# Optimization experiments

Measured on AMD Instinct MI355X. Metric: run time of the kernel, lower is better.

The kernel has to match this reference:

```python
import jax, jax.numpy as jnp
import numpy as np
from jax import lax

B, C, H, W = 4, 256, 64, 64
R1, R2 = 4, 8


def conv1x1(x, w, b):
    # x: [B,C,H,W], w: [O,C], b: [O]
    return jnp.einsum('bchw,oc->bohw', x, w) + b[None, :, None, None]


def dwconv3x3(x, w, b):
    # depthwise 3x3, SAME padding. w: [C,1,3,3]
    y = lax.conv_general_dilated(x, w, window_strides=(1, 1), padding='SAME',
                                 dimension_numbers=('NCHW', 'OIHW', 'NCHW'),
                                 feature_group_count=x.shape[1])
    return y + b[None, :, None, None]


def setup_inputs() -> dict:
    key = jax.random.key(0)
    ks = jax.random.split(key, 20)
    s = 0.02
    inp = {
        'x':   jax.random.normal(ks[0], (B, C, H, W), jnp.float32),
        'Wq':  jax.random.normal(ks[1], (C, C), jnp.float32) * s,
        'bq':  jnp.zeros((C,), jnp.float32),
        'Wk':  jax.random.normal(ks[2], (C, 1, 3, 3), jnp.float32) * s,
        'bk':  jnp.zeros((C,), jnp.float32),
        'Wv':  jax.random.normal(ks[3], (C, 1, 3, 3), jnp.float32) * s,
        'bv':  jnp.zeros((C,), jnp.float32),
        'Wl':  jax.random.normal(ks[4], (C, 1, 3, 3), jnp.float32) * s,
        'bl':  jnp.zeros((C,), jnp.float32),
        'Ws1': jax.random.normal(ks[5], (C // R1, C), jnp.float32) * s,
        'bs1': jnp.zeros((C // R1,), jnp.float32),
        'Ws2': jax.random.normal(ks[6], (C, C // R1), jnp.float32) * s,
        'bs2': jnp.zeros((C,), jnp.float32),
        'Wc1': jax.random.normal(ks[7], (C // R2, C), jnp.float32) * s,
        'bc1': jnp.zeros((C // R2,), jnp.float32),
        'Wc2': jax.random.normal(ks[8], (C, C // R2), jnp.float32) * s,
        'bc2': jnp.zeros((C,), jnp.float32),
        'Wo':  jax.random.normal(ks[9], (C, C), jnp.float32) * s,
        'bo':  jnp.zeros((C,), jnp.float32),
    }
    return inp


def reference(x, Wq, bq, Wk, bk, Wv, bv, Wl, bl, Ws1, bs1, Ws2, bs2,
              Wc1, bc1, Wc2, bc2, Wo, bo):
    b_, c_, h_, w_ = x.shape
    hw = h_ * w_
    scale = jnp.sqrt(jnp.float32(c_))

    q = conv1x1(x, Wq, bq).reshape(b_, c_, hw).transpose(0, 2, 1)   # [B,HW,C]
    k = dwconv3x3(x, Wk, bk).reshape(b_, c_, hw)                    # [B,C,HW]
    v_img = dwconv3x3(x, Wv, bv)                                    # [B,C,H,W]
    v = v_img.reshape(b_, c_, hw).transpose(0, 2, 1)                # [B,HW,C]

    attn = jax.nn.softmax(jnp.einsum('bnc,bcm->bnm', q, k) / scale, axis=-1)
    global_out = jnp.einsum('bnm,bmc->bnc', attn, v)                # [B,HW,C]
    global_out = global_out.transpose(0, 2, 1).reshape(b_, c_, h_, w_)

    local_out = dwconv3x3(v_img, Wl, bl)                            # [B,C,H,W]

    spatial_weight = jax.nn.sigmoid(
        conv1x1(jax.nn.relu(conv1x1(local_out, Ws1, bs1)), Ws2, bs2))

    gap = jnp.mean(global_out, axis=(2, 3), keepdims=True)          # [B,C,1,1]
    channel_weight = jax.nn.sigmoid(
        conv1x1(jax.nn.relu(conv1x1(gap, Wc1, bc1)), Wc2, bc2))     # [B,C,1,1]

    fused = global_out * channel_weight + local_out * spatial_weight
    return conv1x1(fused, Wo, bo) + x
```

## Files before the change

### kernel.cpp

```cpp
#include <hip/hip_runtime.h>
#include <hip/hip_fp8.h>
#include <stdint.h>

typedef unsigned short u16;
typedef unsigned char u8;
typedef __attribute__((ext_vector_type(8))) __bf16 bf16x8;
typedef __attribute__((ext_vector_type(8))) short short8s;
typedef __attribute__((ext_vector_type(4))) float float4v;
typedef __attribute__((ext_vector_type(16))) float floatx16;

static constexpr int NB = 4, NC = 256, NH = 64, NW = 64, NHW = 4096;
static constexpr int BC = 64;
static constexpr int NKV = 4;
static constexpr int KVCHUNK = NHW / NKV;

static constexpr size_t MB = 1ull << 20;
static constexpr size_t OFF_KBF    = 0;
static constexpr size_t OFF_LBF    = 8 * MB;
static constexpr size_t OFF_GT     = 0;
static constexpr size_t OFF_XT     = 16 * MB;
static constexpr size_t OFF_LPART  = 16 * MB;
static constexpr size_t OFF_FUSEDT = 16 * MB;
static constexpr size_t OFF_QT8    = 24 * MB;
static constexpr size_t OFF_KT8    = 32 * MB;
static constexpr size_t OFF_V8     = 40 * MB;
static constexpr size_t OFF_LT     = 48 * MB;
static constexpr size_t OFF_OPART  = 56 * MB;
static constexpr size_t OFF_HIDT   = 88 * MB;
static constexpr size_t OFF_GAP    = OFF_HIDT + 2 * MB;
static constexpr size_t OFF_WQB    = OFF_GAP + 8 * 1024;
static constexpr size_t OFF_WS1B   = OFF_WQB + 131072;
static constexpr size_t OFF_WS2B   = OFF_WS1B + 32768;
static constexpr size_t OFF_WOB    = OFF_WS2B + 32768;

__device__ __forceinline__ float b2f(u16 h) {
    union { float f; unsigned u; } v; v.u = ((unsigned)h) << 16; return v.f;
}
__device__ __forceinline__ u16 f2b(float f) {
    union { float f; unsigned u; } v; v.f = f;
    unsigned r = v.u + 0x7fffu + ((v.u >> 16) & 1u);
    return (u16)(r >> 16);
}
__device__ __forceinline__ u8 f2f8(float f) {
    __hip_fp8_e4m3 h(f);
    return *reinterpret_cast<u8*>(&h);
}

__device__ __forceinline__ void load_lds16(const void* gsrc, void* ldst) {
    __builtin_amdgcn_global_load_lds(
        (__attribute__((address_space(1))) void*)(uintptr_t)gsrc,
        (__attribute__((address_space(3))) void*)ldst,
        16, 0, 0);
}

__global__ __launch_bounds__(256) void prep(
    const float* __restrict__ x,
    const float* __restrict__ Wq, const float* __restrict__ Ws1,
    const float* __restrict__ Ws2, const float* __restrict__ Wo,
    const float* __restrict__ Wk, const float* __restrict__ bk,
    const float* __restrict__ Wv, const float* __restrict__ bv,
    const float* __restrict__ Wl, const float* __restrict__ bl,
    u16* __restrict__ Wqb, u16* __restrict__ Ws1b, u16* __restrict__ Ws2b, u16* __restrict__ Wob,
    float* __restrict__ gap,
    u16* __restrict__ k_bf, u8* __restrict__ vN8, u16* __restrict__ local_bf,
    u16* __restrict__ xT)
{
    __shared__ __align__(16) unsigned char pshm[9216];
    const int bid = blockIdx.x;
    const int t = threadIdx.x;

    if (bid < 644) {
        int id = bid * 256 + t;
        if (id < 65536)        Wqb[id] = f2b(Wq[id]);
        else if (id < 81920)   Ws1b[id - 65536] = f2b(Ws1[id - 65536]);
        else if (id < 98304)   Ws2b[id - 81920] = f2b(Ws2[id - 81920]);
        else if (id < 163840)  Wob[id - 98304] = f2b(Wo[id - 98304]);
        else if (id < 164864)  gap[id - 163840] = 0.f;
        return;
    }
    if (bid < 2692) {
        int l = bid - 644;
        int xx0 = t & 63, cl = t >> 6;
        int y0 = (l & 7) * 8;
        int c  = ((l >> 3) & 63) * 4 + cl;
        int b  = l >> 9;
        const float* xb = x + ((size_t)b * NC + c) * NHW;
        float wk[9], wv[9], wl[9];
#pragma unroll
        for (int i = 0; i < 9; i++) { wk[i] = Wk[c*9+i]; wv[i] = Wv[c*9+i]; wl[i] = Wl[c*9+i]; }
        float bkc = bk[c], bvc = bv[c], blc = bl[c];

        auto ldx = [&](int y) -> float {
            return ((unsigned)y <= 63u) ? xb[y * 64 + xx0] : 0.f;
        };
        auto conv3 = [&](const float* w9, float a, float bm, float cc) -> float {
            float au = __shfl_up(a, 1, 64),   ad = __shfl_down(a, 1, 64);
            float bu = __shfl_up(bm, 1, 64),  bd = __shfl_down(bm, 1, 64);
            float cu = __shfl_up(cc, 1, 64),  cd = __shfl_down(cc, 1, 64);
            float al = (xx0 == 0) ? 0.f : au, ar = (xx0 == 63) ? 0.f : ad;
            float bl_ = (xx0 == 0) ? 0.f : bu, br = (xx0 == 63) ? 0.f : bd;
            float cle = (xx0 == 0) ? 0.f : cu, cr = (xx0 == 63) ? 0.f : cd;
            return w9[0]*al + w9[1]*a  + w9[2]*ar
                 + w9[3]*bl_ + w9[4]*bm + w9[5]*br
                 + w9[6]*cle + w9[7]*cc + w9[8]*cr;
        };

        float xm2 = ldx(y0 - 2), xm1 = ldx(y0 - 1), x0v = ldx(y0), xp1 = ldx(y0 + 1);
        float vm1 = (y0 - 1 >= 0) ? (bvc + conv3(wv, xm2, xm1, x0v)) : 0.f;
        float v0  = bvc + conv3(wv, xm1, x0v, xp1);

        size_t base = ((size_t)b * NC + c) * NHW;
#pragma unroll
        for (int yi = 0; yi < 8; yi++) {
            int y = y0 + yi;
            float xp2 = ldx(y + 2);
            float vp1 = (y + 1 <= 63) ? (bvc + conv3(wv, x0v, xp1, xp2)) : 0.f;
            float kk  = bkc + conv3(wk, xm1, x0v, xp1);
            float ll  = blc + conv3(wl, vm1, v0, vp1);
            size_t o = base + y * 64 + xx0;
            k_bf[o]     = f2b(kk);
            vN8[o]      = f2f8(v0);
            local_bf[o] = f2b(ll);
            xm1 = x0v; x0v = xp1; xp1 = xp2;
            vm1 = v0;  v0 = vp1;
        }
        return;
    }
    {
        u16 (*tile)[72] = reinterpret_cast<u16 (*)[72]>(pshm);
        int l = bid - 2692;
        int n0 = (l & 63) * 64;
        int c0 = ((l >> 6) & 3) * 64;
        int b  = l >> 8;
        const float* src = x + (size_t)b * NC * NHW;
        u16* dst = xT + (size_t)b * NHW * NC;
        int c = t >> 2, nb = (t & 3) * 16;
#pragma unroll
        for (int q = 0; q < 4; q++) {
            float4 v = *(const float4*)(src + (size_t)(c0 + c) * NHW + n0 + nb + q * 4);
            tile[c][nb + q * 4 + 0] = f2b(v.x);
            tile[c][nb + q * 4 + 1] = f2b(v.y);
            tile[c][nb + q * 4 + 2] = f2b(v.z);
            tile[c][nb + q * 4 + 3] = f2b(v.w);
        }
        __syncthreads();
        int cl = t & 63, ng = t >> 6;
#pragma unroll
        for (int j = 0; j < 16; j++) {
            int n = ng * 16 + j;
            dst[(size_t)(n0 + n) * NC + c0 + cl] = tile[cl][n];
        }
    }
}

__global__ __launch_bounds__(256) void mid(
    const u16* __restrict__ k_bf, const u16* __restrict__ local_bf,
    u8* __restrict__ kT8, u16* __restrict__ localT,
    const u16* __restrict__ xT, const u16* __restrict__ Wqb, const float* __restrict__ bq,
    u8* __restrict__ qT8)
{
    __shared__ __align__(16) u16 tile[64][72];
    const int t = threadIdx.x;
    const int bid = blockIdx.x;
    if (bid < 2048) {
        int n0 = (bid & 63) * 64, c0 = ((bid >> 6) & 3) * 64;
        int zb = bid >> 8, b = zb >> 1;
        const u16* src = (zb & 1) ? local_bf : k_bf;
        src += (size_t)b * NC * NHW;
        int c = t >> 2, nb = (t & 3) * 16;
        *(short8s*)&tile[c][nb]     = *(const short8s*)(src + (size_t)(c0 + c) * NHW + n0 + nb);
        *(short8s*)&tile[c][nb + 8] = *(const short8s*)(src + (size_t)(c0 + c) * NHW + n0 + nb + 8);
        __syncthreads();
        int cl = t & 63, ng = t >> 6;
        if (zb & 1) {
            u16* dst = localT + (size_t)b * NHW * NC;
#pragma unroll
            for (int j = 0; j < 16; j++) {
                int n = ng * 16 + j;
                dst[(size_t)(n0 + n) * NC + c0 + cl] = tile[cl][n];
            }
        } else {
            u8* dst = kT8 + (size_t)b * NHW * NC;
#pragma unroll
            for (int j = 0; j < 16; j++) {
                int n = ng * 16 + j;
                dst[(size_t)(n0 + n) * NC + c0 + cl] = f2f8(b2f(tile[cl][n]));
            }
        }
        return;
    }
    {
        const int w = t >> 6, lane = t & 63;
        const int lm = lane & 15, quad = lane >> 4;
        const int l = bid - 2048;
        const int b = l >> 7;
        const int s_base = (l & 127) * 32 + (w & 1) * 16;
        const int ch = (w >> 1) * 128;
        const u16* xTb = xT + (size_t)b * NHW * NC;
        u8* qTb = qT8 + (size_t)b * NHW * NC;
        bf16x8 aq[8];
#pragma unroll
        for (int kt = 0; kt < 8; kt++)
            aq[kt] = *(const bf16x8*)(xTb + (size_t)(s_base + lm) * NC + kt * 32 + quad * 8);
        float4v acc[8];
#pragma unroll
        for (int j = 0; j < 8; j++) acc[j] = (float4v){0.f, 0.f, 0.f, 0.f};
#pragma unroll
        for (int kt = 0; kt < 8; kt++) {
#pragma unroll
            for (int j = 0; j < 8; j++) {
                bf16x8 bw = *(const bf16x8*)(Wqb + (size_t)(ch + j * 16 + lm) * 256 + kt * 32 + quad * 8);
                acc[j] = __builtin_amdgcn_mfma_f32_16x16x32_bf16(aq[kt], bw, acc[j], 0, 0, 0);
            }
        }
#pragma unroll
        for (int j = 0; j < 8; j++) {
            int cout = ch + j * 16 + lm;
            float bb = bq[cout];
#pragma unroll
            for (int r = 0; r < 4; r++) {
                int s = s_base + quad * 4 + r;
                qTb[(size_t)s * NC + cout] = f2f8(acc[j][r] + bb);
            }
        }
    }
}

__device__ __forceinline__ void stage_tiles(
    const u8* __restrict__ kb, const u8* __restrict__ vb8, int kv0,
    u8* KlB, u8* VlB, int w, int lane)
{
#pragma unroll
    for (int i = 0; i < 4; i++) {
        int g = (w * 4 + i) * 64 + lane;
        int n = g >> 4, jj = g & 15, cc = jj ^ (n & 15);
        load_lds16(kb + (size_t)(kv0 + n) * NC + cc * 16, KlB + (w * 4 + i) * 1024);
    }
#pragma unroll
    for (int i = 0; i < 4; i++) {
        int g = (w * 4 + i) * 64 + lane;
        int c = g >> 2, hh = g & 3;
        int sc = hh ^ ((c >> 1) & 3);
        load_lds16(vb8 + (size_t)c * NHW + kv0 + sc * 16, VlB + (w * 4 + i) * 1024);
    }
}

__global__ __launch_bounds__(256, 2) void attn_hid(
    const u8* __restrict__ qT8, const u8* __restrict__ kT8,
    const u8* __restrict__ vN8, u8* __restrict__ Opart8, float* __restrict__ lpart,
    const u16* __restrict__ localT, const u16* __restrict__ Ws1b, const float* __restrict__ bs1,
    u16* __restrict__ hidT)
{
    __shared__ __align__(16) u8 Kl[2][BC * 256];
    __shared__ __align__(16) u8 Vl[2][256 * BC];

    const int t = threadIdx.x;
    const int w = t >> 6, lane = t & 63;

    if (blockIdx.x >= 512) {
        const int lm = lane & 15, quad = lane >> 4;
        const int l = blockIdx.x - 512;
        const int b = l >> 7;
        const int s_base = (l & 127) * 32 + (w & 1) * 16;
        const int ch = (w >> 1) * 32;
        const u16* lTb = localT + (size_t)b * NHW * NC;
        u16* hTb = hidT + (size_t)b * NHW * 64;
        bf16x8 ah[8];
#pragma unroll
        for (int kt = 0; kt < 8; kt++)
            ah[kt] = *(const bf16x8*)(lTb + (size_t)(s_base + lm) * NC + kt * 32 + quad * 8);
        float4v acc[2];
#pragma unroll
        for (int j = 0; j < 2; j++) acc[j] = (float4v){0.f, 0.f, 0.f, 0.f};
#pragma unroll
        for (int kt = 0; kt < 8; kt++) {
#pragma unroll
            for (int j = 0; j < 2; j++) {
                bf16x8 bw = *(const bf16x8*)(Ws1b + (size_t)(ch + j * 16 + lm) * 256 + kt * 32 + quad * 8);
                acc[j] = __builtin_amdgcn_mfma_f32_16x16x32_bf16(ah[kt], bw, acc[j], 0, 0, 0);
            }
        }
#pragma unroll
        for (int j = 0; j < 2; j++) {
            int h = ch + j * 16 + lm;
            float bb = bs1[h];
#pragma unroll
            for (int r = 0; r < 4; r++) {
                int s = s_base + quad * 4 + r;
                hTb[(size_t)s * 64 + h] = f2b(fmaxf(acc[j][r] + bb, 0.0f));
            }
        }
        return;
    }

    const int combo = blockIdx.x & 15;
    const int b  = combo >> 2;
    const int jc = combo & 3;
    const int n0 = (blockIdx.x >> 4) * 128;
    const int lr = lane & 31, l5 = lane >> 5;

    const u8* qb = qT8 + (size_t)b * NHW * NC;
    const u8* kb = kT8 + (size_t)b * NHW * NC;
    const u8* vb8 = vN8 + (size_t)b * NC * NHW;

    long aq[16];
    {
        int qrow = n0 + w * 32 + lr;
#pragma unroll
        for (int kt = 0; kt < 16; kt++)
            aq[kt] = *(const long*)(qb + (size_t)qrow * NC + kt * 16 + l5 * 8);
    }

    floatx16 oacc[8];
#pragma unroll
    for (int i = 0; i < 8; i++)
#pragma unroll
        for (int j = 0; j < 16; j++) oacc[i][j] = 0.f;
    float lsum = 0.f;

    const int kvbeg = jc * KVCHUNK;
    stage_tiles(kb, vb8, kvbeg, Kl[0], Vl[0], w, lane);

    int buf = 0;
#pragma unroll 1
    for (int it = 0; it < KVCHUNK / BC; it++) {
        const int nxt = (it + 1 < KVCHUNK / BC) ? (kvbeg + (it + 1) * BC) : kvbeg;
        stage_tiles(kb, vb8, nxt, Kl[buf ^ 1], Vl[buf ^ 1], w, lane);
        asm volatile("s_waitcnt vmcnt(8)" ::: "memory");
        __builtin_amdgcn_s_barrier();

        const u8* KlB = Kl[buf];
        const u8* VlB = Vl[buf];

#pragma unroll
        for (int s = 0; s < 2; s++) {
            floatx16 sacc;
#pragma unroll
            for (int j = 0; j < 16; j++) sacc[j] = 0.f;
            __builtin_amdgcn_s_setprio(1);
#pragma unroll
            for (int kt = 0; kt < 16; kt++) {
                long ak = *(const long*)&KlB[(s * 32 + lr) * 256 + ((kt ^ (lr & 15)) * 16) + l5 * 8];
                sacc = __builtin_amdgcn_mfma_f32_32x32x16_fp8_fp8(ak, aq[kt], sacc, 0, 0, 0);
            }
            __builtin_amdgcn_s_setprio(0);
            unsigned u0 = 0, u1 = 0, u2 = 0, u3 = 0;
            {
                float p[16];
#pragma unroll
                for (int r = 0; r < 16; r++)
                    p[r] = __expf(sacc[r] * 0.0625f);
                float s0 = (p[0] + p[1]) + (p[2] + p[3]);
                float s1 = (p[4] + p[5]) + (p[6] + p[7]);
                float s2 = (p[8] + p[9]) + (p[10] + p[11]);
                float s3 = (p[12] + p[13]) + (p[14] + p[15]);
                lsum += (s0 + s1) + (s2 + s3);
                u0 = __builtin_amdgcn_cvt_pk_fp8_f32(p[0], p[1], 0, false);
                u0 = __builtin_amdgcn_cvt_pk_fp8_f32(p[2], p[3], u0, true);
                u1 = __builtin_amdgcn_cvt_pk_fp8_f32(p[4], p[5], 0, false);
                u1 = __builtin_amdgcn_cvt_pk_fp8_f32(p[6], p[7], u1, true);
                u2 = __builtin_amdgcn_cvt_pk_fp8_f32(p[8], p[9], 0, false);
                u2 = __builtin_amdgcn_cvt_pk_fp8_f32(p[10], p[11], u2, true);
                u3 = __builtin_amdgcn_cvt_pk_fp8_f32(p[12], p[13], 0, false);
                u3 = __builtin_amdgcn_cvt_pk_fp8_f32(p[14], p[15], u3, true);
            }
            asm volatile("v_permlane32_swap_b32 %0, %1" : "+v"(u0), "+v"(u1));
            asm volatile("v_permlane32_swap_b32 %0, %1" : "+v"(u2), "+v"(u3));
            long A1 = (long)(((unsigned long long)u1 << 32) | u0);
            long A2 = (long)(((unsigned long long)u3 << 32) | u2);

            __builtin_amdgcn_s_setprio(1);
#pragma unroll
            for (int ct = 0; ct < 8; ct++) {
                int c = ct * 32 + lr;
                int sw = (c >> 1) & 3;
                long bv0 = *(const long*)&VlB[c * 64 + (((2 * s) ^ sw) * 16) + l5 * 8];
                long bv1 = *(const long*)&VlB[c * 64 + (((2 * s + 1) ^ sw) * 16) + l5 * 8];
                oacc[ct] = __builtin_amdgcn_mfma_f32_32x32x16_fp8_fp8(A1, bv0, oacc[ct], 0, 0, 0);
                oacc[ct] = __builtin_amdgcn_mfma_f32_32x32x16_fp8_fp8(A2, bv1, oacc[ct], 0, 0, 0);
            }
            __builtin_amdgcn_s_setprio(0);
        }
        __builtin_amdgcn_s_barrier();
        buf ^= 1;
    }

    lsum += __shfl_xor(lsum, 32, 64);
    u8* Ob = Opart8 + ((size_t)(b * NKV + jc) * NHW + n0 + w * 32) * NC;
#pragma unroll
    for (int reg = 0; reg < 16; reg++) {
        int row = (reg & 3) + 8 * (reg >> 2) + 4 * l5;
#pragma unroll
        for (int ct = 0; ct < 8; ct++)
            Ob[(size_t)row * NC + ct * 32 + lr] = f2f8(oacc[ct][reg]);
    }
    if (lane < 32)
        lpart[(size_t)(b * NKV + jc) * NHW + n0 + w * 32 + lr] = lsum;
}

__global__ __launch_bounds__(256) void attn_combine(
    const u8* __restrict__ Opart8, const float* __restrict__ lpart,
    u16* __restrict__ gT, float* __restrict__ gap)
{
    __shared__ float gsum[256];
    int t = threadIdx.x;
    gsum[t] = 0.f;
    __syncthreads();
    int b = blockIdx.y;
    int n = blockIdx.x * 8 + (t >> 5);
    int c0 = (t & 31) * 8;
    float acc[8] = {};
    float l = 0.f;
#pragma unroll
    for (int j = 0; j < NKV; j++) {
        const u8* op = Opart8 + ((size_t)(b * NKV + j) * NHW + n) * NC + c0;
        unsigned long long v = *(const unsigned long long*)op;
        unsigned lo = (unsigned)v, hi = (unsigned)(v >> 32);
        acc[0] += __builtin_amdgcn_cvt_f32_fp8(lo, 0);
        acc[1] += __builtin_amdgcn_cvt_f32_fp8(lo, 1);
        acc[2] += __builtin_amdgcn_cvt_f32_fp8(lo, 2);
        acc[3] += __builtin_amdgcn_cvt_f32_fp8(lo, 3);
        acc[4] += __builtin_amdgcn_cvt_f32_fp8(hi, 0);
        acc[5] += __builtin_amdgcn_cvt_f32_fp8(hi, 1);
        acc[6] += __builtin_amdgcn_cvt_f32_fp8(hi, 2);
        acc[7] += __builtin_amdgcn_cvt_f32_fp8(hi, 3);
        l += lpart[(size_t)(b * NKV + j) * NHW + n];
    }
    float inv = 1.0f / l;
#pragma unroll
    for (int i = 0; i < 8; i++) acc[i] *= inv;
    short8s vo;
#pragma unroll
    for (int i = 0; i < 8; i++) ((u16*)&vo)[i] = f2b(acc[i]);
    *(short8s*)(gT + ((size_t)b * NHW + n) * NC + c0) = vo;
#pragma unroll
    for (int i = 0; i < 8; i++) atomicAdd(&gsum[c0 + i], acc[i]);
    __syncthreads();
    atomicAdd(&gap[b * NC + t], gsum[t]);
}

__global__ __launch_bounds__(256) void gemm_swfused_mfma(
    const u16* __restrict__ hidT, const u16* __restrict__ Ws2b, const float* __restrict__ bs2,
    const u16* __restrict__ gT, const u16* __restrict__ localT,
    const float* __restrict__ gap,
    const float* __restrict__ Wc1, const float* __restrict__ bc1,
    const float* __restrict__ Wc2, const float* __restrict__ bc2,
    u16* __restrict__ fusedT)
{
    __shared__ float g[256], h1[32], cwl[256];
    __shared__ float ph[32][9];
    const int t = threadIdx.x, w = t >> 6, lane = t & 63;
    const int lm = lane & 15, quad = lane >> 4;
    const int b = blockIdx.y;

    g[t] = gap[b * 256 + t] * (1.0f / 4096.0f);
    __syncthreads();
    {
        int h = t & 31, part = t >> 5;
        float s = 0.f;
        for (int c = part * 32; c < part * 32 + 32; c++) s += Wc1[h * 256 + c] * g[c];
        ph[h][part] = s;
    }
    __syncthreads();
    if (t < 32) {
        float s = bc1[t];
#pragma unroll
        for (int p = 0; p < 8; p++) s += ph[t][p];
        h1[t] = fmaxf(s, 0.f);
    }
    __syncthreads();
    {
        float s = bc2[t];
#pragma unroll
        for (int j = 0; j < 32; j++) s += Wc2[t * 32 + j] * h1[j];
        cwl[t] = 1.0f / (1.0f + __expf(-s));
    }
    __syncthreads();

    const int s_base = blockIdx.x * 32 + (w & 1) * 16;
    const int ch = (w >> 1) * 128;
    const u16* hTb = hidT + (size_t)b * NHW * 64;
    const u16* lTb = localT + (size_t)b * NHW * NC;
    const u16* gTb = gT + (size_t)b * NHW * NC;
    u16* fTb = fusedT + (size_t)b * NHW * NC;

    bf16x8 aq[2];
#pragma unroll
    for (int kt = 0; kt < 2; kt++)
        aq[kt] = *(const bf16x8*)(hTb + (size_t)(s_base + lm) * 64 + kt * 32 + quad * 8);

    float4v acc[8];
#pragma unroll
    for (int j = 0; j < 8; j++) acc[j] = (float4v){0.f, 0.f, 0.f, 0.f};

#pragma unroll
    for (int kt = 0; kt < 2; kt++) {
#pragma unroll
        for (int j = 0; j < 8; j++) {
            bf16x8 bw = *(const bf16x8*)(Ws2b + (size_t)(ch + j * 16 + lm) * 64 + kt * 32 + quad * 8);
            acc[j] = __builtin_amdgcn_mfma_f32_16x16x32_bf16(aq[kt], bw, acc[j], 0, 0, 0);
        }
    }
#pragma unroll
    for (int j = 0; j < 8; j++) {
        int c = ch + j * 16 + lm;
        float bb = bs2[c];
        float cwv = cwl[c];
#pragma unroll
        for (int r = 0; r < 4; r++) {
            int s = s_base + quad * 4 + r;
            float sw = 1.0f / (1.0f + __expf(-(acc[j][r] + bb)));
            float gg = b2f(gTb[(size_t)s * NC + c]);
            float lo = b2f(lTb[(size_t)s * NC + c]);
            fTb[(size_t)s * NC + c] = f2b(gg * cwv + lo * sw);
        }
    }
}

__global__ __launch_bounds__(256) void gemm_out_mfma(
    const u16* __restrict__ Wob, const u16* __restrict__ fusedT, const float* __restrict__ bo,
    const float* __restrict__ x, float* __restrict__ out)
{
    const int t = threadIdx.x, w = t >> 6, lane = t & 63;
    const int lm = lane & 15, quad = lane >> 4;
    const int b = blockIdx.z;
    const int o_base = blockIdx.x * 32 + (w & 1) * 16;
    const int n_base = blockIdx.y * 256 + (w >> 1) * 128;
    const u16* fTb = fusedT + (size_t)b * NHW * NC;

    bf16x8 aw[8];
#pragma unroll
    for (int kt = 0; kt < 8; kt++)
        aw[kt] = *(const bf16x8*)(Wob + (size_t)(o_base + lm) * 256 + kt * 32 + quad * 8);

    float4v acc[8];
#pragma unroll
    for (int j = 0; j < 8; j++) acc[j] = (float4v){0.f, 0.f, 0.f, 0.f};

#pragma unroll
    for (int kt = 0; kt < 8; kt++) {
#pragma unroll
        for (int j = 0; j < 8; j++) {
            bf16x8 bf = *(const bf16x8*)(fTb + (size_t)(n_base + j * 16 + lm) * NC + kt * 32 + quad * 8);
            acc[j] = __builtin_amdgcn_mfma_f32_16x16x32_bf16(aw[kt], bf, acc[j], 0, 0, 0);
        }
    }
#pragma unroll
    for (int r = 0; r < 4; r++) {
        int o = o_base + quad * 4 + r;
        float bb = bo[o];
        size_t rowoff = ((size_t)b * NC + o) * NHW;
#pragma unroll
        for (int j = 0; j < 8; j++) {
            int n = n_base + j * 16 + lm;
            out[rowoff + n] = acc[j][r] + bb + x[rowoff + n];
        }
    }
}

extern "C" void kernel_launch(void* const* d_in, const int* in_sizes, int n_in,
                              void* d_out, int out_size, void* d_ws, size_t ws_size,
                              hipStream_t stream)
{
    const float* x   = (const float*)d_in[0];
    const float* Wq  = (const float*)d_in[1];
    const float* bq  = (const float*)d_in[2];
    const float* Wk  = (const float*)d_in[3];
    const float* bk  = (const float*)d_in[4];
    const float* Wv  = (const float*)d_in[5];
    const float* bv  = (const float*)d_in[6];
    const float* Wl  = (const float*)d_in[7];
    const float* bl  = (const float*)d_in[8];
    const float* Ws1 = (const float*)d_in[9];
    const float* bs1 = (const float*)d_in[10];
    const float* Ws2 = (const float*)d_in[11];
    const float* bs2 = (const float*)d_in[12];
    const float* Wc1 = (const float*)d_in[13];
    const float* bc1 = (const float*)d_in[14];
    const float* Wc2 = (const float*)d_in[15];
    const float* bc2 = (const float*)d_in[16];
    const float* Wo  = (const float*)d_in[17];
    const float* bo  = (const float*)d_in[18];
    float* out = (float*)d_out;

    char* ws = (char*)d_ws;
    u16* k_bf     = (u16*)(ws + OFF_KBF);
    u16* local_bf = (u16*)(ws + OFF_LBF);
    u16* gT       = (u16*)(ws + OFF_GT);
    u16* xT       = (u16*)(ws + OFF_XT);
    u16* fusedT   = (u16*)(ws + OFF_FUSEDT);
    u8*  qT8      = (u8*)(ws + OFF_QT8);
    u8*  kT8      = (u8*)(ws + OFF_KT8);
    u8*  vN8      = (u8*)(ws + OFF_V8);
    u16* localT   = (u16*)(ws + OFF_LT);
    u8*  Opart8   = (u8*)(ws + OFF_OPART);
    float* lpart  = (float*)(ws + OFF_LPART);
    u16* hidT     = (u16*)(ws + OFF_HIDT);
    float* gap    = (float*)(ws + OFF_GAP);
    u16* Wqb      = (u16*)(ws + OFF_WQB);
    u16* Ws1b     = (u16*)(ws + OFF_WS1B);
    u16* Ws2b     = (u16*)(ws + OFF_WS2B);
    u16* Wob      = (u16*)(ws + OFF_WOB);

    prep<<<dim3(3716), 256, 0, stream>>>(x, Wq, Ws1, Ws2, Wo, Wk, bk, Wv, bv, Wl, bl,
                                         Wqb, Ws1b, Ws2b, Wob, gap, k_bf, vN8, local_bf, xT);
    mid<<<dim3(2560), 256, 0, stream>>>(k_bf, local_bf, kT8, localT, xT, Wqb, bq, qT8);
    attn_hid<<<dim3(1024), 256, 0, stream>>>(qT8, kT8, vN8, Opart8, lpart,
                                             localT, Ws1b, bs1, hidT);
    attn_combine<<<dim3(NHW / 8, 4), 256, 0, stream>>>(Opart8, lpart, gT, gap);
    gemm_swfused_mfma<<<dim3(128, 4), 256, 0, stream>>>(hidT, Ws2b, bs2, gT, localT,
                                                        gap, Wc1, bc1, Wc2, bc2, fusedT);
    gemm_out_mfma<<<dim3(8, 16, 4), 256, 0, stream>>>(Wob, fusedT, bo, x, out);
}
```

Measured before the change: 274.3 us.

## Use scaled 32x32x64 fp8 MFMA for attention QK and PV products

New measurement: 259.9 us. 5.3% less time.

```diff
diff --git a/kernel.cpp b/kernel.cpp
--- a/kernel.cpp
+++ b/kernel.cpp
@@ -8,6 +8,8 @@
 typedef __attribute__((ext_vector_type(8))) short short8s;
 typedef __attribute__((ext_vector_type(4))) float float4v;
 typedef __attribute__((ext_vector_type(16))) float floatx16;
+typedef __attribute__((ext_vector_type(4))) int int4v;
+typedef __attribute__((ext_vector_type(8))) int int8v;
 
 static constexpr int NB = 4, NC = 256, NH = 64, NW = 64, NHW = 4096;
 static constexpr int BC = 64;
@@ -298,17 +300,19 @@
     const int jc = combo & 3;
     const int n0 = (blockIdx.x >> 4) * 128;
     const int lr = lane & 31, l5 = lane >> 5;
+    const int m4 = lr & 15;
+    const int scl = (int)0x7F7F7F7F;
 
     const u8* qb = qT8 + (size_t)b * NHW * NC;
     const u8* kb = kT8 + (size_t)b * NHW * NC;
     const u8* vb8 = vN8 + (size_t)b * NC * NHW;
 
-    long aq[16];
+    int8v aqm[4];
     {
         int qrow = n0 + w * 32 + lr;
 #pragma unroll
-        for (int kt = 0; kt < 16; kt++)
-            aq[kt] = *(const long*)(qb + (size_t)qrow * NC + kt * 16 + l5 * 8);
+        for (int ks = 0; ks < 4; ks++)
+            aqm[ks] = *(const int8v*)(qb + (size_t)qrow * NC + ks * 64 + l5 * 32);
     }
 
     floatx16 oacc[8];
@@ -332,55 +336,93 @@
         const u8* KlB = Kl[buf];
         const u8* VlB = Vl[buf];
 
-#pragma unroll
-        for (int s = 0; s < 2; s++) {
+        unsigned uA0, uA1, uA2, uA3, uB0, uB1, uB2, uB3;
+
+        {
             floatx16 sacc;
 #pragma unroll
             for (int j = 0; j < 16; j++) sacc[j] = 0.f;
             __builtin_amdgcn_s_setprio(1);
 #pragma unroll
-            for (int kt = 0; kt < 16; kt++) {
-                long ak = *(const long*)&KlB[(s * 32 + lr) * 256 + ((kt ^ (lr & 15)) * 16) + l5 * 8];
-                sacc = __builtin_amdgcn_mfma_f32_32x32x16_fp8_fp8(ak, aq[kt], sacc, 0, 0, 0);
+            for (int ks = 0; ks < 4; ks++) {
+                int e = ks * 4 + l5 * 2;
+                int4v klo = *(const int4v*)&KlB[lr * 256 + ((e ^ m4) * 16)];
+                int4v khi = *(const int4v*)&KlB[lr * 256 + (((e + 1) ^ m4) * 16)];
+                int8v ka = __builtin_shufflevector(klo, khi, 0, 1, 2, 3, 4, 5, 6, 7);
+                sacc = __builtin_amdgcn_mfma_scale_f32_32x32x64_f8f6f4(
+                    ka, aqm[ks], sacc, 0, 0, 0, scl, 0, scl);
             }
             __builtin_amdgcn_s_setprio(0);
-            unsigned u0 = 0, u1 = 0, u2 = 0, u3 = 0;
-            {
-                float p[16];
-#pragma unroll
-                for (int r = 0; r < 16; r++)
-                    p[r] = __expf(sacc[r] * 0.0625f);
-                float s0 = (p[0] + p[1]) + (p[2] + p[3]);
-                float s1 = (p[4] + p[5]) + (p[6] + p[7]);
-                float s2 = (p[8] + p[9]) + (p[10] + p[11]);
-                float s3 = (p[12] + p[13]) + (p[14] + p[15]);
-                lsum += (s0 + s1) + (s2 + s3);
-                u0 = __builtin_amdgcn_cvt_pk_fp8_f32(p[0], p[1], 0, false);
-                u0 = __builtin_amdgcn_cvt_pk_fp8_f32(p[2], p[3], u0, true);
-                u1 = __builtin_amdgcn_cvt_pk_fp8_f32(p[4], p[5], 0, false);
-                u1 = __builtin_amdgcn_cvt_pk_fp8_f32(p[6], p[7], u1, true);
-                u2 = __builtin_amdgcn_cvt_pk_fp8_f32(p[8], p[9], 0, false);
-                u2 = __builtin_amdgcn_cvt_pk_fp8_f32(p[10], p[11], u2, true);
-                u3 = __builtin_amdgcn_cvt_pk_fp8_f32(p[12], p[13], 0, false);
-                u3 = __builtin_amdgcn_cvt_pk_fp8_f32(p[14], p[15], u3, true);
-            }
-            asm volatile("v_permlane32_swap_b32 %0, %1" : "+v"(u0), "+v"(u1));
-            asm volatile("v_permlane32_swap_b32 %0, %1" : "+v"(u2), "+v"(u3));
-            long A1 = (long)(((unsigned long long)u1 << 32) | u0);
-            long A2 = (long)(((unsigned long long)u3 << 32) | u2);
-
+            float p[16];
+#pragma unroll
+            for (int r = 0; r < 16; r++)
+                p[r] = __expf(sacc[r] * 0.0625f);
+            float s0 = (p[0] + p[1]) + (p[2] + p[3]);
+            float s1 = (p[4] + p[5]) + (p[6] + p[7]);
+            float s2 = (p[8] + p[9]) + (p[10] + p[11]);
+            float s3 = (p[12] + p[13]) + (p[14] + p[15]);
+            lsum += (s0 + s1) + (s2 + s3);
+            uA0 = __builtin_amdgcn_cvt_pk_fp8_f32(p[0], p[1], 0, false);
+            uA0 = __builtin_amdgcn_cvt_pk_fp8_f32(p[2], p[3], uA0, true);
+            uA1 = __builtin_amdgcn_cvt_pk_fp8_f32(p[4], p[5], 0, false);
+            uA1 = __builtin_amdgcn_cvt_pk_fp8_f32(p[6], p[7], uA1, true);
+            uA2 = __builtin_amdgcn_cvt_pk_fp8_f32(p[8], p[9], 0, false);
+            uA2 = __builtin_amdgcn_cvt_pk_fp8_f32(p[10], p[11], uA2, true);
+            uA3 = __builtin_amdgcn_cvt_pk_fp8_f32(p[12], p[13], 0, false);
+            uA3 = __builtin_amdgcn_cvt_pk_fp8_f32(p[14], p[15], uA3, true);
+        }
+        {
+            floatx16 sacc;
+#pragma unroll
+            for (int j = 0; j < 16; j++) sacc[j] = 0.f;
             __builtin_amdgcn_s_setprio(1);
 #pragma unroll
-            for (int ct = 0; ct < 8; ct++) {
-                int c = ct * 32 + lr;
-                int sw = (c >> 1) & 3;
-                long bv0 = *(const long*)&VlB[c * 64 + (((2 * s) ^ sw) * 16) + l5 * 8];
-                long bv1 = *(const long*)&VlB[c * 64 + (((2 * s + 1) ^ sw) * 16) + l5 * 8];
-                oacc[ct] = __builtin_amdgcn_mfma_f32_32x32x16_fp8_fp8(A1, bv0, oacc[ct], 0, 0, 0);
-                oacc[ct] = __builtin_amdgcn_mfma_f32_32x32x16_fp8_fp8(A2, bv1, oacc[ct], 0, 0, 0);
+            for (int ks = 0; ks < 4; ks++) {
+                int e = ks * 4 + l5 * 2;
+                int4v klo = *(const int4v*)&KlB[(32 + lr) * 256 + ((e ^ m4) * 16)];
+                int4v khi = *(const int4v*)&KlB[(32 + lr) * 256 + (((e + 1) ^ m4) * 16)];
+                int8v ka = __builtin_shufflevector(klo, khi, 0, 1, 2, 3, 4, 5, 6, 7);
+                sacc = __builtin_amdgcn_mfma_scale_f32_32x32x64_f8f6f4(
+                    ka, aqm[ks], sacc, 0, 0, 0, scl, 0, scl);
             }
             __builtin_amdgcn_s_setprio(0);
-        }
+            float p[16];
+#pragma unroll
+            for (int r = 0; r < 16; r++)
+                p[r] = __expf(sacc[r] * 0.0625f);
+            float s0 = (p[0] + p[1]) + (p[2] + p[3]);
+            float s1 = (p[4] + p[5]) + (p[6] + p[7]);
+            float s2 = (p[8] + p[9]) + (p[10] + p[11]);
+            float s3 = (p[12] + p[13]) + (p[14] + p[15]);
+            lsum += (s0 + s1) + (s2 + s3);
+            uB0 = __builtin_amdgcn_cvt_pk_fp8_f32(p[0], p[1], 0, false);
+            uB0 = __builtin_amdgcn_cvt_pk_fp8_f32(p[2], p[3], uB0, true);
+            uB1 = __builtin_amdgcn_cvt_pk_fp8_f32(p[4], p[5], 0, false);
+            uB1 = __builtin_amdgcn_cvt_pk_fp8_f32(p[6], p[7], uB1, true);
+            uB2 = __builtin_amdgcn_cvt_pk_fp8_f32(p[8], p[9], 0, false);
+            uB2 = __builtin_amdgcn_cvt_pk_fp8_f32(p[10], p[11], uB2, true);
+            uB3 = __builtin_amdgcn_cvt_pk_fp8_f32(p[12], p[13], 0, false);
+            uB3 = __builtin_amdgcn_cvt_pk_fp8_f32(p[14], p[15], uB3, true);
+        }
+        asm volatile("v_permlane32_swap_b32 %0, %1" : "+v"(uA0), "+v"(uB0));
+        asm volatile("v_permlane32_swap_b32 %0, %1" : "+v"(uA1), "+v"(uB1));
+        asm volatile("v_permlane32_swap_b32 %0, %1" : "+v"(uA2), "+v"(uB2));
+        asm volatile("v_permlane32_swap_b32 %0, %1" : "+v"(uA3), "+v"(uB3));
+        int8v pa = {(int)uA0, (int)uB0, (int)uA1, (int)uB1,
+                    (int)uA2, (int)uB2, (int)uA3, (int)uB3};
+
+        __builtin_amdgcn_s_setprio(1);
+#pragma unroll
+        for (int ct = 0; ct < 8; ct++) {
+            int c = ct * 32 + lr;
+            int sw = (c >> 1) & 3;
+            int4v v0 = *(const int4v*)&VlB[c * 64 + (((l5 * 2) ^ sw) * 16)];
+            int4v v1 = *(const int4v*)&VlB[c * 64 + (((l5 * 2 + 1) ^ sw) * 16)];
+            int8v bv = __builtin_shufflevector(v0, v1, 0, 1, 2, 3, 4, 5, 6, 7);
+            oacc[ct] = __builtin_amdgcn_mfma_scale_f32_32x32x64_f8f6f4(
+                pa, bv, oacc[ct], 0, 0, 0, scl, 0, scl);
+        }
+        __builtin_amdgcn_s_setprio(0);
         __builtin_amdgcn_s_barrier();
         buf ^= 1;
     }
```
